# Kernel optimization log

Hardware: AMD Instinct MI355X
Metric: run time of the kernel (lower is better)

Reference implementation:

```python
import jax, jax.numpy as jnp
import numpy as np

HEADS = 12
ROPE_THETA = 10000.0

def _rope(t):
    # t: [B, H, N, D]; lucidrains interleaved RoPE (rotate_half over adjacent pairs)
    B, H, N, D = t.shape
    inv_freq = 1.0 / (ROPE_THETA ** (jnp.arange(0, D, 2, dtype=jnp.float32) / D))  # [D/2]
    freqs = jnp.arange(N, dtype=jnp.float32)[:, None] * inv_freq[None, :]          # [N, D/2]
    freqs = jnp.repeat(freqs, 2, axis=-1)                                          # [N, D]
    cos, sin = jnp.cos(freqs), jnp.sin(freqs)
    tp = t.reshape(B, H, N, D // 2, 2)
    rot = jnp.stack([-tp[..., 1], tp[..., 0]], axis=-1).reshape(B, H, N, D)
    return t * cos + rot * sin

def setup_inputs() -> dict:
    key = jax.random.key(0)
    k1, k2, k3 = jax.random.split(key, 3)
    dim = 768
    x = jax.random.normal(k1, (2, 2048, dim), dtype=jnp.float32)
    w_qkv = jax.random.normal(k2, (3 * dim, dim), dtype=jnp.float32) * (dim ** -0.5)
    w_proj = jax.random.normal(k3, (dim, dim), dtype=jnp.float32) * (dim ** -0.5)
    b_proj = jnp.zeros((dim,), dtype=jnp.float32)
    return {"x": x, "w_qkv": w_qkv, "w_proj": w_proj, "b_proj": b_proj}

def reference(x, w_qkv, w_proj, b_proj):
    B, N, C = x.shape
    H = HEADS
    d = C // H
    scale = d ** -0.5
    qkv = x @ w_qkv.T                                # [B, N, 3C]
    q, k, v = jnp.split(qkv, 3, axis=-1)
    def to_heads(t):
        return t.reshape(B, N, H, d).transpose(0, 2, 1, 3)  # [B,H,N,d]
    q, k, v = map(to_heads, (q, k, v))
    q = _rope(q * scale)
    k = _rope(k)
    attn = jnp.einsum('bhid,bhjd->bhij', q, k)
    attn = jax.nn.softmax(attn, axis=-1)
    out = jnp.einsum('bhij,bhjd->bhid', attn, v)
    out = out.transpose(0, 2, 1, 3).reshape(B, N, C)
    return out @ w_proj.T + b_proj
```

## Files before the change

### kernel.cpp

```cpp
#include <hip/hip_runtime.h>
#include <math.h>

#define NSEQ 2048
#define CDIM 768
#define NH   12
#define HD   64
#define NB   2

typedef unsigned short u16;
typedef __attribute__((ext_vector_type(8))) short bf16x8;
typedef __attribute__((ext_vector_type(4))) float f32x4;
typedef __attribute__((ext_vector_type(8))) float f32x8;
typedef __attribute__((ext_vector_type(4))) __bf16 bf16x4t;
typedef __attribute__((ext_vector_type(8))) __bf16 bf16x8t;

__device__ __forceinline__ u16 f2bf(float x) {
    unsigned int u = __float_as_uint(x);
    u += 0x7fffu + ((u >> 16) & 1u);
    return (u16)(u >> 16);
}

__device__ __forceinline__ uint4 pack8(float4 a, float4 b) {
    f32x8 v = {a.x, a.y, a.z, a.w, b.x, b.y, b.z, b.w};
    union { bf16x8t t; uint4 u; } o;
    o.t = __builtin_convertvector(v, bf16x8t);
    return o.u;
}

#define LSTR 72

#define GLD16(gp, lp) __builtin_amdgcn_global_load_lds( \
    (__attribute__((address_space(1))) void*)(const void*)(gp), \
    (__attribute__((address_space(3))) void*)(void*)(lp), 16, 0, 0)

__global__ __launch_bounds__(256)
void qkv_mfma_kernel(const float* __restrict__ Xf, const float* __restrict__ Wf,
                     u16* __restrict__ Qb, u16* __restrict__ Kb,
                     u16* __restrict__ Vb)
{
    __shared__ __align__(16) u16 S[2 * 128 * LSTR];
    u16* As = S;
    u16* Bs = S + 128 * LSTR;

    const int tid  = threadIdx.x;
    const int lane = tid & 63;
    const int wid  = tid >> 6;
    const int l15  = lane & 15;
    const int quad = lane >> 4;
    const int wr = wid >> 1, wc = wid & 1;
    const int m0 = blockIdx.x * 128;
    const int n0 = blockIdx.y * 128;

    const int row = tid >> 3, c8s = (tid & 7) << 3;

    f32x4 acc[4][4];
#pragma unroll
    for (int mi = 0; mi < 4; ++mi)
#pragma unroll
        for (int ni = 0; ni < 4; ++ni)
            acc[mi][ni] = (f32x4){0.f, 0.f, 0.f, 0.f};

    float4 pa[4][2], pb[4][2];
#pragma unroll
    for (int it = 0; it < 4; ++it) {
        size_t ga = (size_t)(m0 + row + 32 * it) * CDIM + c8s;
        size_t gb = (size_t)(n0 + row + 32 * it) * CDIM + c8s;
        pa[it][0] = *(const float4*)&Xf[ga];
        pa[it][1] = *(const float4*)&Xf[ga + 4];
        pb[it][0] = *(const float4*)&Wf[gb];
        pb[it][1] = *(const float4*)&Wf[gb + 4];
    }

    for (int kt = 0; kt < CDIM; kt += 64) {
        __syncthreads();
#pragma unroll
        for (int it = 0; it < 4; ++it) {
            *(uint4*)&As[(row + 32 * it) * LSTR + c8s] =
                pack8(pa[it][0], pa[it][1]);
            *(uint4*)&Bs[(row + 32 * it) * LSTR + c8s] =
                pack8(pb[it][0], pb[it][1]);
        }
        __syncthreads();

        if (kt + 64 < CDIM) {
#pragma unroll
            for (int it = 0; it < 4; ++it) {
                size_t ga = (size_t)(m0 + row + 32 * it) * CDIM + kt + 64 + c8s;
                size_t gb = (size_t)(n0 + row + 32 * it) * CDIM + kt + 64 + c8s;
                pa[it][0] = *(const float4*)&Xf[ga];
                pa[it][1] = *(const float4*)&Xf[ga + 4];
                pb[it][0] = *(const float4*)&Wf[gb];
                pb[it][1] = *(const float4*)&Wf[gb + 4];
            }
        }

#pragma unroll
        for (int k = 0; k < 2; ++k) {
            bf16x8 af[4];
#pragma unroll
            for (int mi = 0; mi < 4; ++mi)
                af[mi] = *(const bf16x8*)
                    &As[(wr * 64 + mi * 16 + l15) * LSTR + quad * 8 + 32 * k];
#pragma unroll
            for (int ni = 0; ni < 4; ++ni) {
                bf16x8 bfr = *(const bf16x8*)
                    &Bs[(wc * 64 + ni * 16 + l15) * LSTR + quad * 8 + 32 * k];
#pragma unroll
                for (int mi = 0; mi < 4; ++mi)
                    acc[mi][ni] = __builtin_amdgcn_mfma_f32_16x16x32_bf16(
                        af[mi], bfr, acc[mi][ni], 0, 0, 0);
            }
        }
    }

    __syncthreads();

    const int bi      = m0 >> 11;
    const int nbase   = (m0 & 2047) + wr * 64;
    const int colbase = n0 + wc * 64;
    const int sel     = colbase / CDIM;
    const int h       = (colbase % CDIM) >> 6;

    u16* Ew = S + wid * 64 * LSTR;
    const int grow = lane >> 3;
    const int gc8  = (lane & 7) << 3;

    if (sel == 2) {
#pragma unroll
        for (int ni = 0; ni < 4; ++ni)
#pragma unroll
            for (int mi = 0; mi < 4; ++mi)
#pragma unroll
                for (int r = 0; r < 4; ++r)
                    Ew[(ni * 16 + l15) * LSTR + mi * 16 + quad * 4 + r] =
                        f2bf(acc[mi][ni][r]);
        u16* dst = Vb + (size_t)(bi * NH + h) * HD * NSEQ;
#pragma unroll
        for (int it = 0; it < 8; ++it) {
            int dd = grow + 8 * it;
            *(uint4*)&dst[(size_t)dd * NSEQ + nbase + gc8] =
                *(const uint4*)&Ew[dd * LSTR + gc8];
        }
    } else {
        u16* dst = ((sel == 0) ? Qb : Kb) + (size_t)(bi * NH + h) * NSEQ * HD;
        const float scl = (sel == 0) ? 0.125f : 1.0f;
#pragma unroll
        for (int ni = 0; ni < 4; ++ni) {
            int dd = ni * 16 + l15;
            float invf = expf(-0.14391156831212787f * (float)(dd & ~1));
#pragma unroll
            for (int mi = 0; mi < 4; ++mi) {
                f32x4 val = acc[mi][ni];
#pragma unroll
                for (int r = 0; r < 4; ++r) {
                    float e = val[r] * scl;
                    float p = __shfl_xor(e, 1);
                    int n = nbase + mi * 16 + quad * 4 + r;
                    float sv, cv;
                    __sincosf((float)n * invf, &sv, &cv);
                    float o = (dd & 1) ? (e * cv + p * sv)
                                       : (e * cv - p * sv);
                    Ew[(mi * 16 + quad * 4 + r) * LSTR + dd] = f2bf(o);
                }
            }
        }
#pragma unroll
        for (int it = 0; it < 8; ++it) {
            int tr = grow + 8 * it;
            *(uint4*)&dst[(size_t)(nbase + tr) * HD + gc8] =
                *(const uint4*)&Ew[tr * LSTR + gc8];
        }
    }
}

#define STAGE_KV(BUF, kt_) do {                                               \
    GLD16(Kg + ((size_t)(((kt_) << 6) + r0) * HD + cs),                       \
          &Ks[BUF][wid * 512]);                                               \
    GLD16(Kg + ((size_t)(((kt_) << 6) + r0 + 32) * HD + cs),                  \
          &Ks[BUF][wid * 512 + 2048]);                                        \
    GLD16(Vg + ((size_t)r0 * NSEQ + ((kt_) << 6) + cs),                       \
          &Vs[BUF][wid * 512]);                                               \
    GLD16(Vg + ((size_t)(r0 + 32) * NSEQ + ((kt_) << 6) + cs),                \
          &Vs[BUF][wid * 512 + 2048]);                                        \
} while (0)

#define ATTN_STEP(kt_, CUR, NXT) do {                                         \
    if ((kt_) + 1 < NSEQ / 64) STAGE_KV(NXT, (kt_) + 1);                      \
    f32x4 sacc[4];                                                            \
    _Pragma("unroll")                                                         \
    for (int mt = 0; mt < 4; ++mt) sacc[mt] = (f32x4){0.f, 0.f, 0.f, 0.f};    \
    _Pragma("unroll")                                                         \
    for (int k = 0; k < 2; ++k) {                                             \
        _Pragma("unroll")                                                     \
        for (int mt = 0; mt < 4; ++mt) {                                      \
            bf16x8 ak = *(const bf16x8*)                                      \
                &Ks[CUR][(mt * 16 + l15) * 64 + ((quad * 8 + 32 * k) ^ swz)]; \
            sacc[mt] = __builtin_amdgcn_mfma_f32_16x16x32_bf16(               \
                ak, aq[k], sacc[mt], 0, 0, 0);                                \
        }                                                                     \
    }                                                                         \
    _Pragma("unroll")                                                         \
    for (int mt = 0; mt < 4; ++mt) {                                          \
        f32x4 ev;                                                             \
        _Pragma("unroll")                                                     \
        for (int r = 0; r < 4; ++r) ev[r] = __expf(sacc[mt][r]);              \
        bf16x4t pbk = __builtin_convertvector(ev, bf16x4t);                   \
        *(bf16x4t*)&Pw[l15 * 64 + ((mt * 16 + quad * 4) ^ swz)] = pbk;        \
    }                                                                         \
    _Pragma("unroll")                                                         \
    for (int k = 0; k < 2; ++k) {                                             \
        bf16x8 ap = *(const bf16x8*)                                          \
            &Pw[l15 * 64 + ((quad * 8 + 32 * k) ^ swz)];                      \
        lacc = __builtin_amdgcn_mfma_f32_16x16x32_bf16(                       \
            ap, vone, lacc, 0, 0, 0);                                         \
        _Pragma("unroll")                                                     \
        for (int t = 0; t < 4; ++t) {                                         \
            bf16x8 bv = *(const bf16x8*)                                      \
                &Vs[CUR][(t * 16 + l15) * 64 + ((quad * 8 + 32 * k) ^ swz)];  \
            O[t] = __builtin_amdgcn_mfma_f32_16x16x32_bf16(                   \
                ap, bv, O[t], 0, 0, 0);                                       \
        }                                                                     \
    }                                                                         \
    __syncthreads();                                                          \
} while (0)

__global__ __launch_bounds__(256)
void attn_kernel(const u16* __restrict__ Qb, const u16* __restrict__ Kb,
                 const u16* __restrict__ Vt, u16* __restrict__ AO)
{
    __shared__ __align__(16) u16 Ks[2][64 * 64];
    __shared__ __align__(16) u16 Vs[2][64 * 64];
    __shared__ __align__(16) u16 Ps[4][16 * 64];

    const int tid  = threadIdx.x;
    const int lane = tid & 63;
    const int wid  = tid >> 6;
    const int l15  = lane & 15;
    const int quad = lane >> 4;
    const int swz  = (l15 & 7) << 3;
    const int qt = blockIdx.x;
    const int bh = blockIdx.y;

    const u16* Qg = Qb + ((size_t)bh * NSEQ + qt * 64) * HD;
    const u16* Kg = Kb + (size_t)bh * NSEQ * HD;
    const u16* Vg = Vt + (size_t)bh * HD * NSEQ;

    const int r0 = tid >> 3;
    const int cs = ((tid & 7) ^ (r0 & 7)) << 3;

    bf16x8 aq[2];
    aq[0] = *(const bf16x8*)&Qg[(wid * 16 + l15) * HD + quad * 8];
    aq[1] = *(const bf16x8*)&Qg[(wid * 16 + l15) * HD + quad * 8 + 32];

    union { u16 s[8]; bf16x8 v; } oneu;
#pragma unroll
    for (int i = 0; i < 8; ++i) oneu.s[i] = 0x3f80;
    const bf16x8 vone = oneu.v;

    f32x4 O[4];
#pragma unroll
    for (int t = 0; t < 4; ++t) O[t] = (f32x4){0.f, 0.f, 0.f, 0.f};
    f32x4 lacc = (f32x4){0.f, 0.f, 0.f, 0.f};

    u16* Pw = Ps[wid];

    STAGE_KV(0, 0);
    __syncthreads();

    for (int kt = 0; kt < NSEQ / 64; kt += 2) {
        ATTN_STEP(kt, 0, 1);
        ATTN_STEP(kt + 1, 1, 0);
    }

    float inv4[4];
#pragma unroll
    for (int r = 0; r < 4; ++r) inv4[r] = 1.0f / lacc[r];

    const int b = bh / NH, h = bh % NH;
#pragma unroll
    for (int r = 0; r < 4; ++r) {
        size_t row = (size_t)b * NSEQ + qt * 64 + wid * 16 + quad * 4 + r;
#pragma unroll
        for (int t = 0; t < 4; ++t)
            AO[row * CDIM + h * HD + t * 16 + l15] = f2bf(O[t][r] * inv4[r]);
    }
}

__global__ __launch_bounds__(256)
void proj_kernel(const u16* __restrict__ A, const float* __restrict__ Wf,
                 const float* __restrict__ bias, float* __restrict__ out)
{
    __shared__ __align__(16) u16 As[64 * 64];
    __shared__ __align__(16) u16 Bs[64 * 64];
    const int tid  = threadIdx.x;
    const int lane = tid & 63;
    const int wid  = tid >> 6;
    const int l15  = lane & 15;
    const int quad = lane >> 4;
    const int swz  = (l15 & 7) << 3;
    const int wr = wid >> 1, wc = wid & 1;
    const int m0 = blockIdx.x * 64;
    const int n0 = blockIdx.y * 64;

    const int r0 = tid >> 3;
    const int cs = ((tid & 7) ^ (r0 & 7)) << 3;
    const int c8 = (tid & 7) << 3;
    const int bswz = c8 ^ ((r0 & 7) << 3);

    f32x4 acc[2][2];
#pragma unroll
    for (int mi = 0; mi < 2; ++mi)
#pragma unroll
        for (int ni = 0; ni < 2; ++ni)
            acc[mi][ni] = (f32x4){0.f, 0.f, 0.f, 0.f};

    for (int kt = 0; kt < CDIM; kt += 64) {
        __syncthreads();
        GLD16(A + ((size_t)(m0 + r0) * CDIM + kt + cs),      &As[wid * 512]);
        GLD16(A + ((size_t)(m0 + r0 + 32) * CDIM + kt + cs), &As[wid * 512 + 2048]);
        {
            size_t gb0 = (size_t)(n0 + r0) * CDIM + kt + c8;
            size_t gb1 = (size_t)(n0 + r0 + 32) * CDIM + kt + c8;
            float4 w0 = *(const float4*)&Wf[gb0];
            float4 w1 = *(const float4*)&Wf[gb0 + 4];
            float4 w2 = *(const float4*)&Wf[gb1];
            float4 w3 = *(const float4*)&Wf[gb1 + 4];
            *(uint4*)&Bs[r0 * 64 + bswz]        = pack8(w0, w1);
            *(uint4*)&Bs[(r0 + 32) * 64 + bswz] = pack8(w2, w3);
        }
        __syncthreads();

#pragma unroll
        for (int k = 0; k < 2; ++k) {
            bf16x8 af[2], bf[2];
#pragma unroll
            for (int mi = 0; mi < 2; ++mi)
                af[mi] = *(const bf16x8*)
                    &As[(wr * 32 + mi * 16 + l15) * 64 + ((quad * 8 + 32 * k) ^ swz)];
#pragma unroll
            for (int ni = 0; ni < 2; ++ni)
                bf[ni] = *(const bf16x8*)
                    &Bs[(wc * 32 + ni * 16 + l15) * 64 + ((quad * 8 + 32 * k) ^ swz)];
#pragma unroll
            for (int mi = 0; mi < 2; ++mi)
#pragma unroll
                for (int ni = 0; ni < 2; ++ni)
                    acc[mi][ni] = __builtin_amdgcn_mfma_f32_16x16x32_bf16(
                        af[mi], bf[ni], acc[mi][ni], 0, 0, 0);
        }
    }

#pragma unroll
    for (int ni = 0; ni < 2; ++ni) {
        int col = n0 + wc * 32 + ni * 16 + l15;
        float bb = bias[col];
#pragma unroll
        for (int mi = 0; mi < 2; ++mi) {
            int row = m0 + wr * 32 + mi * 16 + quad * 4;
#pragma unroll
            for (int r = 0; r < 4; ++r)
                out[(size_t)(row + r) * CDIM + col] = acc[mi][ni][r] + bb;
        }
    }
}

extern "C" void kernel_launch(void* const* d_in, const int* in_sizes, int n_in,
                              void* d_out, int out_size, void* d_ws,
                              size_t ws_size, hipStream_t stream)
{
    const float* X     = (const float*)d_in[0];
    const float* Wqkv  = (const float*)d_in[1];
    const float* Wproj = (const float*)d_in[2];
    const float* bias  = (const float*)d_in[3];
    float* out = (float*)d_out;

    const size_t per_buf = (size_t)NB * NH * NSEQ * HD;
    u16* Qb  = (u16*)d_ws;
    u16* Kb  = Qb + per_buf;
    u16* Vb  = Kb + per_buf;
    u16* AOb = Vb + per_buf;

    qkv_mfma_kernel<<<dim3(32, 18), 256, 0, stream>>>(X, Wqkv, Qb, Kb, Vb);
    attn_kernel<<<dim3(32, 24), 256, 0, stream>>>(Qb, Kb, Vb, AOb);
    proj_kernel<<<dim3(64, 12), 256, 0, stream>>>(AOb, Wproj, bias, out);
}
```

Measured before the change: 161.6 us.

## Shrink QKV tile to 128x64 and remap block order for XCD locality

The QKV GEMM tile shrinks from 128x128 to 128x64, doubling the grid to 1152 blocks, and a 1D grid is remapped so that consecutive blocks on each of the 8 XCDs share input rows. The attention kernel gets a matching 1D-grid remap that groups the heads each XCD handles, so K/V tiles are reused in that XCD's L2. The V transpose epilogue now stages through shared memory for the whole block, with an extra barrier. Smaller tiles improve occupancy and load balance across CUs but reduce per-block reuse of X.

```diff
diff --git a/kernel.cpp b/kernel.cpp
--- a/kernel.cpp
+++ b/kernel.cpp
@@ -28,6 +28,7 @@
 }
 
 #define LSTR 72
+#define ESTR 136
 
 #define GLD16(gp, lp) __builtin_amdgcn_global_load_lds( \
     (__attribute__((address_space(1))) void*)(const void*)(gp), \
@@ -38,7 +39,7 @@
                      u16* __restrict__ Qb, u16* __restrict__ Kb,
                      u16* __restrict__ Vb)
 {
-    __shared__ __align__(16) u16 S[2 * 128 * LSTR];
+    __shared__ __align__(16) u16 S[(128 + 64) * LSTR];
     u16* As = S;
     u16* Bs = S + 128 * LSTR;
 
@@ -47,26 +48,31 @@
     const int wid  = tid >> 6;
     const int l15  = lane & 15;
     const int quad = lane >> 4;
-    const int wr = wid >> 1, wc = wid & 1;
-    const int m0 = blockIdx.x * 128;
-    const int n0 = blockIdx.y * 128;
+
+    const int f  = blockIdx.x;
+    const int L  = (f & 7) * 144 + (f >> 3);
+    const int m0 = (L / 36) * 128;
+    const int n0 = (L % 36) * 64;
 
     const int row = tid >> 3, c8s = (tid & 7) << 3;
 
-    f32x4 acc[4][4];
-#pragma unroll
-    for (int mi = 0; mi < 4; ++mi)
+    f32x4 acc[2][4];
+#pragma unroll
+    for (int mi = 0; mi < 2; ++mi)
 #pragma unroll
         for (int ni = 0; ni < 4; ++ni)
             acc[mi][ni] = (f32x4){0.f, 0.f, 0.f, 0.f};
 
-    float4 pa[4][2], pb[4][2];
+    float4 pa[4][2], pb[2][2];
 #pragma unroll
     for (int it = 0; it < 4; ++it) {
         size_t ga = (size_t)(m0 + row + 32 * it) * CDIM + c8s;
-        size_t gb = (size_t)(n0 + row + 32 * it) * CDIM + c8s;
         pa[it][0] = *(const float4*)&Xf[ga];
         pa[it][1] = *(const float4*)&Xf[ga + 4];
+    }
+#pragma unroll
+    for (int it = 0; it < 2; ++it) {
+        size_t gb = (size_t)(n0 + row + 32 * it) * CDIM + c8s;
         pb[it][0] = *(const float4*)&Wf[gb];
         pb[it][1] = *(const float4*)&Wf[gb + 4];
     }
@@ -74,21 +80,25 @@
     for (int kt = 0; kt < CDIM; kt += 64) {
         __syncthreads();
 #pragma unroll
-        for (int it = 0; it < 4; ++it) {
+        for (int it = 0; it < 4; ++it)
             *(uint4*)&As[(row + 32 * it) * LSTR + c8s] =
                 pack8(pa[it][0], pa[it][1]);
+#pragma unroll
+        for (int it = 0; it < 2; ++it)
             *(uint4*)&Bs[(row + 32 * it) * LSTR + c8s] =
                 pack8(pb[it][0], pb[it][1]);
-        }
         __syncthreads();
 
         if (kt + 64 < CDIM) {
 #pragma unroll
             for (int it = 0; it < 4; ++it) {
                 size_t ga = (size_t)(m0 + row + 32 * it) * CDIM + kt + 64 + c8s;
-                size_t gb = (size_t)(n0 + row + 32 * it) * CDIM + kt + 64 + c8s;
                 pa[it][0] = *(const float4*)&Xf[ga];
                 pa[it][1] = *(const float4*)&Xf[ga + 4];
+            }
+#pragma unroll
+            for (int it = 0; it < 2; ++it) {
+                size_t gb = (size_t)(n0 + row + 32 * it) * CDIM + kt + 64 + c8s;
                 pb[it][0] = *(const float4*)&Wf[gb];
                 pb[it][1] = *(const float4*)&Wf[gb + 4];
             }
@@ -96,17 +106,17 @@
 
 #pragma unroll
         for (int k = 0; k < 2; ++k) {
-            bf16x8 af[4];
-#pragma unroll
-            for (int mi = 0; mi < 4; ++mi)
+            bf16x8 af[2];
+#pragma unroll
+            for (int mi = 0; mi < 2; ++mi)
                 af[mi] = *(const bf16x8*)
-                    &As[(wr * 64 + mi * 16 + l15) * LSTR + quad * 8 + 32 * k];
+                    &As[(wid * 32 + mi * 16 + l15) * LSTR + quad * 8 + 32 * k];
 #pragma unroll
             for (int ni = 0; ni < 4; ++ni) {
                 bf16x8 bfr = *(const bf16x8*)
-                    &Bs[(wc * 64 + ni * 16 + l15) * LSTR + quad * 8 + 32 * k];
-#pragma unroll
-                for (int mi = 0; mi < 4; ++mi)
+                    &Bs[(ni * 16 + l15) * LSTR + quad * 8 + 32 * k];
+#pragma unroll
+                for (int mi = 0; mi < 2; ++mi)
                     acc[mi][ni] = __builtin_amdgcn_mfma_f32_16x16x32_bf16(
                         af[mi], bfr, acc[mi][ni], 0, 0, 0);
             }
@@ -116,40 +126,41 @@
     __syncthreads();
 
     const int bi      = m0 >> 11;
-    const int nbase   = (m0 & 2047) + wr * 64;
-    const int colbase = n0 + wc * 64;
-    const int sel     = colbase / CDIM;
-    const int h       = (colbase % CDIM) >> 6;
-
-    u16* Ew = S + wid * 64 * LSTR;
-    const int grow = lane >> 3;
-    const int gc8  = (lane & 7) << 3;
+    const int tokbase = m0 & 2047;
+    const int nbase   = tokbase + wid * 32;
+    const int sel     = n0 / CDIM;
+    const int h       = (n0 % CDIM) >> 6;
 
     if (sel == 2) {
+        u16* Ew = S;
 #pragma unroll
         for (int ni = 0; ni < 4; ++ni)
 #pragma unroll
-            for (int mi = 0; mi < 4; ++mi)
+            for (int mi = 0; mi < 2; ++mi)
 #pragma unroll
                 for (int r = 0; r < 4; ++r)
-                    Ew[(ni * 16 + l15) * LSTR + mi * 16 + quad * 4 + r] =
-                        f2bf(acc[mi][ni][r]);
+                    Ew[(ni * 16 + l15) * ESTR + wid * 32 + mi * 16 + quad * 4 + r]
+                        = f2bf(acc[mi][ni][r]);
+        __syncthreads();
         u16* dst = Vb + (size_t)(bi * NH + h) * HD * NSEQ;
 #pragma unroll
-        for (int it = 0; it < 8; ++it) {
-            int dd = grow + 8 * it;
-            *(uint4*)&dst[(size_t)dd * NSEQ + nbase + gc8] =
-                *(const uint4*)&Ew[dd * LSTR + gc8];
+        for (int it = 0; it < 4; ++it) {
+            int idx = tid + 256 * it;
+            int dd  = idx >> 4;
+            int c8  = (idx & 15) << 3;
+            *(uint4*)&dst[(size_t)dd * NSEQ + tokbase + c8] =
+                *(const uint4*)&Ew[dd * ESTR + c8];
         }
     } else {
         u16* dst = ((sel == 0) ? Qb : Kb) + (size_t)(bi * NH + h) * NSEQ * HD;
         const float scl = (sel == 0) ? 0.125f : 1.0f;
+        u16* Ew = S + wid * 32 * LSTR;
 #pragma unroll
         for (int ni = 0; ni < 4; ++ni) {
             int dd = ni * 16 + l15;
             float invf = expf(-0.14391156831212787f * (float)(dd & ~1));
 #pragma unroll
-            for (int mi = 0; mi < 4; ++mi) {
+            for (int mi = 0; mi < 2; ++mi) {
                 f32x4 val = acc[mi][ni];
 #pragma unroll
                 for (int r = 0; r < 4; ++r) {
@@ -165,8 +176,10 @@
             }
         }
 #pragma unroll
-        for (int it = 0; it < 8; ++it) {
-            int tr = grow + 8 * it;
+        for (int it = 0; it < 4; ++it) {
+            int ch  = lane + 64 * it;
+            int tr  = ch >> 3;
+            int gc8 = (ch & 7) << 3;
             *(uint4*)&dst[(size_t)(nbase + tr) * HD + gc8] =
                 *(const uint4*)&Ew[tr * LSTR + gc8];
         }
@@ -238,8 +251,11 @@
     const int l15  = lane & 15;
     const int quad = lane >> 4;
     const int swz  = (l15 & 7) << 3;
-    const int qt = blockIdx.x;
-    const int bh = blockIdx.y;
+
+    const int f  = blockIdx.x;
+    const int i  = f >> 3;
+    const int bh = (f & 7) * 3 + (i >> 5);
+    const int qt = i & 31;
 
     const u16* Qg = Qb + ((size_t)bh * NSEQ + qt * 64) * HD;
     const u16* Kg = Kb + (size_t)bh * NSEQ * HD;
@@ -254,7 +270,7 @@
 
     union { u16 s[8]; bf16x8 v; } oneu;
 #pragma unroll
-    for (int i = 0; i < 8; ++i) oneu.s[i] = 0x3f80;
+    for (int ii = 0; ii < 8; ++ii) oneu.s[ii] = 0x3f80;
     const bf16x8 vone = oneu.v;
 
     f32x4 O[4];
@@ -279,10 +295,10 @@
     const int b = bh / NH, h = bh % NH;
 #pragma unroll
     for (int r = 0; r < 4; ++r) {
-        size_t row = (size_t)b * NSEQ + qt * 64 + wid * 16 + quad * 4 + r;
+        size_t orow = (size_t)b * NSEQ + qt * 64 + wid * 16 + quad * 4 + r;
 #pragma unroll
         for (int t = 0; t < 4; ++t)
-            AO[row * CDIM + h * HD + t * 16 + l15] = f2bf(O[t][r] * inv4[r]);
+            AO[orow * CDIM + h * HD + t * 16 + l15] = f2bf(O[t][r] * inv4[r]);
     }
 }
 
@@ -356,10 +372,10 @@
         float bb = bias[col];
 #pragma unroll
         for (int mi = 0; mi < 2; ++mi) {
-            int row = m0 + wr * 32 + mi * 16 + quad * 4;
+            int rw = m0 + wr * 32 + mi * 16 + quad * 4;
 #pragma unroll
             for (int r = 0; r < 4; ++r)
-                out[(size_t)(row + r) * CDIM + col] = acc[mi][ni][r] + bb;
+                out[(size_t)(rw + r) * CDIM + col] = acc[mi][ni][r] + bb;
         }
     }
 }
@@ -380,7 +396,7 @@
     u16* Vb  = Kb + per_buf;
     u16* AOb = Vb + per_buf;
 
-    qkv_mfma_kernel<<<dim3(32, 18), 256, 0, stream>>>(X, Wqkv, Qb, Kb, Vb);
-    attn_kernel<<<dim3(32, 24), 256, 0, stream>>>(Qb, Kb, Vb, AOb);
+    qkv_mfma_kernel<<<dim3(1152), 256, 0, stream>>>(X, Wqkv, Qb, Kb, Vb);
+    attn_kernel<<<dim3(768), 256, 0, stream>>>(Qb, Kb, Vb, AOb);
     proj_kernel<<<dim3(64, 12), 256, 0, stream>>>(AOb, Wproj, bias, out);
 }
```

Measured after the change: 162.2 us. Within noise of the previous version (+0.4%).
